# Kernel optimization log

Hardware: AMD Instinct MI355X
Metric: run time of the kernel (lower is better)

## Reference

```python
import jax, jax.numpy as jnp
import numpy as np
import math

PHI = (1.0 + math.sqrt(5.0)) / 2.0
LUT_SIZE = 4096
TWO_PI = 2.0 * math.pi


def _lut_tables():
    # 4096-entry sin/cos lookup tables over [0, 2*pi)
    grid = jnp.arange(LUT_SIZE, dtype=jnp.float32) * (TWO_PI / LUT_SIZE)
    return jnp.sin(grid), jnp.cos(grid)


def _lookup_sin_cos(theta, sin_t, cos_t):
    # nearest-entry LUT lookup: index = round(theta / (2*pi) * N) mod N
    idx = jnp.mod(jnp.round(theta * (LUT_SIZE / TWO_PI)), LUT_SIZE).astype(jnp.int32)
    return sin_t[idx], cos_t[idx]


def setup_inputs() -> dict:
    key = jax.random.key(0)
    ks = jax.random.split(key, 6)
    B, D, H = 16, 2048, 2048
    return {
        "current_state_real": jax.random.normal(ks[0], (B, D), jnp.float32),
        "current_state_imag": jax.random.normal(ks[1], (B, D), jnp.float32),
        "history_real": jax.random.normal(ks[2], (B, H, D), jnp.float32),
        "history_imag": jax.random.normal(ks[3], (B, H, D), jnp.float32),
        "ema_state": jax.random.normal(ks[4], (B, 2 * D), jnp.float32),
        "w_q": jax.random.normal(ks[5], (D,), jnp.float32) * 0.02,
        "b_q": jnp.zeros((D,), jnp.float32),
        "alpha": jnp.asarray(0.1, jnp.float32),
        "t": jnp.asarray(3.0, jnp.float32),
    }


def reference(current_state_real, current_state_imag, history_real, history_imag,
              ema_state, w_q, b_q, alpha, t):
    D = current_state_real.shape[-1]
    scale = math.sqrt(2.0 * D)
    sin_t, cos_t = _lut_tables()

    wl_q = 1.0 + jnp.abs(w_q)                      # (D,)
    t_phi = t * PHI
    theta_real = current_state_real / wl_q + b_q + t_phi   # (B, D)
    theta_imag = current_state_imag / wl_q + b_q + t_phi   # (B, D)
    _, cos_q_real = _lookup_sin_cos(theta_real, sin_t, cos_t)
    _, cos_q_imag = _lookup_sin_cos(theta_imag, sin_t, cos_t)

    # keys == values == stacked history (no projection): (B, H, 2D)
    keys = jnp.concatenate([history_real, history_imag], axis=-1)
    query_for_match = jnp.concatenate([cos_q_real, cos_q_imag], axis=-1)  # (B, 2D)

    scores = jnp.einsum('bd,bhd->bh', query_for_match, keys) / scale      # (B, H)
    weights = jax.nn.softmax(scores, axis=-1)
    retrieved = jnp.einsum('bh,bhd->bd', weights, keys)                   # (B, 2D)

    a = jax.nn.sigmoid(alpha)
    new_ema = a * retrieved + (1.0 - a) * ema_state
    return new_ema
```

## Files before the change

### kernel.cpp

```cpp
#include <hip/hip_runtime.h>
#include <math.h>

#ifndef M_PI
#define M_PI 3.14159265358979323846
#endif

#define LUT_N 4096
#define WPB 4

__device__ __forceinline__ float lut_cos(float theta) {
    const float IDX_SCALE = (float)((double)LUT_N / (2.0 * M_PI));
    const float STEP = (float)((2.0 * M_PI) / (double)LUT_N);
    float x = theta * IDX_SCALE;
    int i = (int)rintf(x);
    i &= (LUT_N - 1);
    return cosf((float)i * STEP);
}

__global__ void qgen_kernel(const float* __restrict__ cur_r,
                            const float* __restrict__ cur_i,
                            const float* __restrict__ w_q,
                            const float* __restrict__ b_q,
                            const float* __restrict__ t_ptr,
                            float* __restrict__ q_out,
                            int B, int D) {
    int idx = blockIdx.x * blockDim.x + threadIdx.x;
    int twoD = 2 * D;
    if (idx >= B * twoD) return;
    int b = idx / twoD;
    int c = idx - b * twoD;
    int col = (c < D) ? c : c - D;
    const float* src = (c < D) ? cur_r : cur_i;
    float v = src[(size_t)b * D + col];
    float t_phi = t_ptr[0] * 1.61803398874989484820f;
    float wl = 1.0f + fabsf(w_q[col]);
    float theta = v / wl + b_q[col] + t_phi;
    q_out[idx] = lut_cos(theta);
}

__global__ __launch_bounds__(256, 2) void flash_kernel(
    const float* __restrict__ hist_r,
    const float* __restrict__ hist_i,
    const float* __restrict__ q_ws,
    float* __restrict__ r_ws,
    float* __restrict__ ml_ws,
    int H, int S) {
    const int t = threadIdx.x;
    const int lane = t & 63;
    const int wv = t >> 6;
    const int b = blockIdx.x / S;
    const int s = blockIdx.x - b * S;
    const int rows_blk = H / S;
    const int R = rows_blk / WPB;
    const int h0 = s * rows_blk + wv * R;

    const float4* hr = (const float4*)hist_r + ((size_t)b * H + h0) * 512;
    const float4* hi = (const float4*)hist_i + ((size_t)b * H + h0) * 512;
    const float4* q4 = (const float4*)q_ws + (size_t)b * 1024;

    float4 qv[16];
#pragma unroll
    for (int j = 0; j < 16; ++j) qv[j] = q4[j * 64 + lane];

    float4 rv[16];
#pragma unroll
    for (int j = 0; j < 16; ++j) rv[j] = make_float4(0.f, 0.f, 0.f, 0.f);
    float m0 = -INFINITY, l = 0.f;
    const float inv_scale = 1.0f / 64.0f;

    for (int r = 0; r < R; ++r) {
        float4 kv[16];
#pragma unroll
        for (int j = 0; j < 8; ++j) kv[j] = hr[(size_t)r * 512 + j * 64 + lane];
#pragma unroll
        for (int j = 0; j < 8; ++j) kv[8 + j] = hi[(size_t)r * 512 + j * 64 + lane];

        float p = 0.f;
#pragma unroll
        for (int j = 0; j < 16; ++j)
            p += qv[j].x * kv[j].x + qv[j].y * kv[j].y +
                 qv[j].z * kv[j].z + qv[j].w * kv[j].w;
#pragma unroll
        for (int off = 32; off; off >>= 1) p += __shfl_xor(p, off);
        float sc = p * inv_scale;

        float d = sc - m0;
        float w;
        if (d > 8.0f) {
            float corr = __expf(-d);
            l *= corr;
#pragma unroll
            for (int j = 0; j < 16; ++j) {
                rv[j].x *= corr; rv[j].y *= corr;
                rv[j].z *= corr; rv[j].w *= corr;
            }
            m0 = sc;
            w = 1.0f;
        } else {
            w = __expf(d);
        }
        l += w;
#pragma unroll
        for (int j = 0; j < 16; ++j) {
            rv[j].x = fmaf(w, kv[j].x, rv[j].x);
            rv[j].y = fmaf(w, kv[j].y, rv[j].y);
            rv[j].z = fmaf(w, kv[j].z, rv[j].z);
            rv[j].w = fmaf(w, kv[j].w, rv[j].w);
        }
    }

    __shared__ float4 sred[1024];
    __shared__ float sm[WPB], sl[WPB];
    if (lane == 0) { sm[wv] = m0; sl[wv] = l; }
    __syncthreads();
    float M = fmaxf(fmaxf(sm[0], sm[1]), fmaxf(sm[2], sm[3]));
    float Lb = sl[0] * __expf(sm[0] - M) + sl[1] * __expf(sm[1] - M) +
               sl[2] * __expf(sm[2] - M) + sl[3] * __expf(sm[3] - M);
    float scale = __expf(m0 - M);

    for (int w = 0; w < WPB; ++w) {
        if (wv == w) {
#pragma unroll
            for (int j = 0; j < 16; ++j) {
                int idx = j * 64 + lane;
                float4 v = (w == 0) ? make_float4(0.f, 0.f, 0.f, 0.f) : sred[idx];
                v.x = fmaf(scale, rv[j].x, v.x);
                v.y = fmaf(scale, rv[j].y, v.y);
                v.z = fmaf(scale, rv[j].z, v.z);
                v.w = fmaf(scale, rv[j].w, v.w);
                sred[idx] = v;
            }
        }
        __syncthreads();
    }

    float4* ro = (float4*)r_ws + (size_t)blockIdx.x * 1024;
#pragma unroll
    for (int k = 0; k < 4; ++k) ro[t + 256 * k] = sred[t + 256 * k];
    if (t == 0) {
        ml_ws[2 * (size_t)blockIdx.x] = M;
        ml_ws[2 * (size_t)blockIdx.x + 1] = Lb;
    }
}

__global__ void combine_kernel(const float* __restrict__ r_ws,
                               const float* __restrict__ ml_ws,
                               const float* __restrict__ ema,
                               const float* __restrict__ alpha_ptr,
                               float* __restrict__ out,
                               int D, int S) {
    const int twoD = 2 * D;
    const int nc = twoD / 256;
    const int b = blockIdx.x / nc;
    const int cb = blockIdx.x - b * nc;
    const int c = cb * 256 + threadIdx.x;

    const float* ml = ml_ws + (size_t)b * S * 2;
    float M = -INFINITY;
    for (int s = 0; s < S; ++s) M = fmaxf(M, ml[2 * s]);
    float L = 0.f;
    for (int s = 0; s < S; ++s) L += ml[2 * s + 1] * __expf(ml[2 * s] - M);

    float acc = 0.f;
    const float* rb = r_ws + (size_t)b * S * twoD + c;
    for (int s = 0; s < S; ++s)
        acc = fmaf(__expf(ml[2 * s] - M), rb[(size_t)s * twoD], acc);

    float a = 1.0f / (1.0f + __expf(-alpha_ptr[0]));
    float retrieved = acc / L;
    size_t o = (size_t)b * twoD + c;
    out[o] = a * retrieved + (1.0f - a) * ema[o];
}

extern "C" void kernel_launch(void* const* d_in, const int* in_sizes, int n_in,
                              void* d_out, int out_size, void* d_ws, size_t ws_size,
                              hipStream_t stream) {
    const float* cur_r  = (const float*)d_in[0];
    const float* cur_i  = (const float*)d_in[1];
    const float* hist_r = (const float*)d_in[2];
    const float* hist_i = (const float*)d_in[3];
    const float* ema    = (const float*)d_in[4];
    const float* w_q    = (const float*)d_in[5];
    const float* b_q    = (const float*)d_in[6];
    const float* alpha  = (const float*)d_in[7];
    const float* t      = (const float*)d_in[8];

    const int D = in_sizes[5];
    const int B = in_sizes[0] / D;
    const int H = in_sizes[2] / (B * D);
    const int twoD = 2 * D;

    float* q_ws = (float*)d_ws;
    size_t q_elems = (size_t)B * twoD;

    int S = 32;
    while (S > 1) {
        size_t need = (q_elems + (size_t)B * S * twoD + (size_t)B * S * 2) * sizeof(float);
        if (need <= ws_size) break;
        S >>= 1;
    }
    float* r_ws = q_ws + q_elems;
    float* ml_ws = r_ws + (size_t)B * S * twoD;

    int qblocks = (B * twoD + 255) / 256;
    qgen_kernel<<<qblocks, 256, 0, stream>>>(cur_r, cur_i, w_q, b_q, t, q_ws, B, D);
    flash_kernel<<<B * S, 256, 0, stream>>>(hist_r, hist_i, q_ws, r_ws, ml_ws, H, S);
    combine_kernel<<<B * (twoD / 256), 256, 0, stream>>>(r_ws, ml_ws, ema, alpha,
                                                         (float*)d_out, D, S);
}
```

Measured before the change: 126.3 us.

## Double-buffer history rows into LDS via async global_load_lds

The flash kernel now stages each wave's next history row into a double-buffered LDS tile with async global-to-LDS loads while it computes on the current row, instead of reading directly from global memory into registers. Row assignment changes from contiguous per-wave chunks to interleaved rows across the four waves, with a block-wide barrier each iteration. The 128KB LDS buffer forces occupancy down to one block per CU, and the extra barrier plus LDS round trip add cost in exchange for hiding load latency. The reduction buffer reuses the staging LDS.

New measurement: 129.6 us. 2.6% more time.

```diff
diff --git a/kernel.cpp b/kernel.cpp
--- a/kernel.cpp
+++ b/kernel.cpp
@@ -7,6 +7,7 @@
 
 #define LUT_N 4096
 #define WPB 4
+#define TROWS 4
 
 __device__ __forceinline__ float lut_cos(float theta) {
     const float IDX_SCALE = (float)((double)LUT_N / (2.0 * M_PI));
@@ -38,7 +39,25 @@
     q_out[idx] = lut_cos(theta);
 }
 
-__global__ __launch_bounds__(256, 2) void flash_kernel(
+typedef const __attribute__((address_space(1))) unsigned int guint;
+typedef __attribute__((address_space(3))) unsigned int suint;
+
+__device__ __forceinline__ void stage_row(const float* __restrict__ hr_row,
+                                          const float* __restrict__ hi_row,
+                                          float* lds_row, int lane) {
+#pragma unroll
+    for (int c = 0; c < 8; ++c)
+        __builtin_amdgcn_global_load_lds(
+            (guint*)(const void*)(hr_row + c * 256 + lane * 4),
+            (suint*)(void*)(lds_row + c * 256), 16, 0, 0);
+#pragma unroll
+    for (int c = 0; c < 8; ++c)
+        __builtin_amdgcn_global_load_lds(
+            (guint*)(const void*)(hi_row + c * 256 + lane * 4),
+            (suint*)(void*)(lds_row + 2048 + c * 256), 16, 0, 0);
+}
+
+__global__ __launch_bounds__(256, 1) void flash_kernel(
     const float* __restrict__ hist_r,
     const float* __restrict__ hist_i,
     const float* __restrict__ q_ws,
@@ -51,13 +70,16 @@
     const int b = blockIdx.x / S;
     const int s = blockIdx.x - b * S;
     const int rows_blk = H / S;
-    const int R = rows_blk / WPB;
-    const int h0 = s * rows_blk + wv * R;
-
-    const float4* hr = (const float4*)hist_r + ((size_t)b * H + h0) * 512;
-    const float4* hi = (const float4*)hist_i + ((size_t)b * H + h0) * 512;
+    const int NT = rows_blk / TROWS;
+
+    __shared__ float buf[2][TROWS][4096];
+    __shared__ float sm[WPB], sl[WPB];
+
+    const size_t row0 = (size_t)b * H + (size_t)s * rows_blk + wv;
+    const float* hr_w = hist_r + row0 * 2048;
+    const float* hi_w = hist_i + row0 * 2048;
+
     const float4* q4 = (const float4*)q_ws + (size_t)b * 1024;
-
     float4 qv[16];
 #pragma unroll
     for (int j = 0; j < 16; ++j) qv[j] = q4[j * 64 + lane];
@@ -68,12 +90,19 @@
     float m0 = -INFINITY, l = 0.f;
     const float inv_scale = 1.0f / 64.0f;
 
-    for (int r = 0; r < R; ++r) {
+    stage_row(hr_w, hi_w, &buf[0][wv][0], lane);
+    __syncthreads();
+
+    for (int kt = 0; kt < NT; ++kt) {
+        if (kt + 1 < NT)
+            stage_row(hr_w + (size_t)(kt + 1) * TROWS * 2048,
+                      hi_w + (size_t)(kt + 1) * TROWS * 2048,
+                      &buf[(kt + 1) & 1][wv][0], lane);
+
+        const float4* krow = (const float4*)&buf[kt & 1][wv][0];
         float4 kv[16];
 #pragma unroll
-        for (int j = 0; j < 8; ++j) kv[j] = hr[(size_t)r * 512 + j * 64 + lane];
-#pragma unroll
-        for (int j = 0; j < 8; ++j) kv[8 + j] = hi[(size_t)r * 512 + j * 64 + lane];
+        for (int j = 0; j < 16; ++j) kv[j] = krow[j * 64 + lane];
 
         float p = 0.f;
 #pragma unroll
@@ -107,10 +136,10 @@
             rv[j].z = fmaf(w, kv[j].z, rv[j].z);
             rv[j].w = fmaf(w, kv[j].w, rv[j].w);
         }
-    }
-
-    __shared__ float4 sred[1024];
-    __shared__ float sm[WPB], sl[WPB];
+
+        __syncthreads();
+    }
+
     if (lane == 0) { sm[wv] = m0; sl[wv] = l; }
     __syncthreads();
     float M = fmaxf(fmaxf(sm[0], sm[1]), fmaxf(sm[2], sm[3]));
@@ -118,6 +147,7 @@
                sl[2] * __expf(sm[2] - M) + sl[3] * __expf(sm[3] - M);
     float scale = __expf(m0 - M);
 
+    float4* sred = (float4*)&buf[0][0][0];
     for (int w = 0; w < WPB; ++w) {
         if (wv == w) {
 #pragma unroll
```
